# Kernel optimization log

Hardware: AMD Instinct MI355X
Metric: run time of the kernel (lower is better)

Reference implementation:

```python
import jax, jax.numpy as jnp
import numpy as np

DIM = 256
HEADS = 4
DEPTH = DIM // HEADS
EXPAND = 4
EPS = 1e-3  # keras BatchNormalization default epsilon


def _bn(x, gamma, beta, mean, var):
    # inference-mode batch norm over last axis
    return gamma * (x - mean) * jax.lax.rsqrt(var + EPS) + beta


def setup_inputs() -> dict:
    key = jax.random.key(0)
    ks = jax.random.split(key, 12)
    B, S, D = 4, 2048, DIM
    H = D * EXPAND
    s = 1.0 / np.sqrt(D)
    inp = {
        "x": jax.random.normal(ks[0], (B, S, D), jnp.float32),
        "bn1_gamma": jnp.ones((D,), jnp.float32),
        "bn1_beta": jnp.zeros((D,), jnp.float32),
        "bn1_mean": jax.random.normal(ks[1], (D,), jnp.float32) * 0.1,
        "bn1_var": jnp.abs(jax.random.normal(ks[2], (D,), jnp.float32)) + 0.5,
        "wq": jax.random.normal(ks[3], (D, D), jnp.float32) * s,
        "bq": jnp.zeros((D,), jnp.float32),
        "wk": jax.random.normal(ks[4], (D, D), jnp.float32) * s,
        "bk": jnp.zeros((D,), jnp.float32),
        "wv": jax.random.normal(ks[5], (D, D), jnp.float32) * s,
        "bv": jnp.zeros((D,), jnp.float32),
        "wo": jax.random.normal(ks[6], (D, D), jnp.float32) * s,
        "bo": jnp.zeros((D,), jnp.float32),
        "bn2_gamma": jnp.ones((D,), jnp.float32),
        "bn2_beta": jnp.zeros((D,), jnp.float32),
        "bn2_mean": jax.random.normal(ks[7], (D,), jnp.float32) * 0.1,
        "bn2_var": jnp.abs(jax.random.normal(ks[8], (D,), jnp.float32)) + 0.5,
        "w1": jax.random.normal(ks[9], (D, H), jnp.float32) * s,
        "w2": jax.random.normal(ks[10], (H, D), jnp.float32) * (1.0 / np.sqrt(H)),
    }
    return inp


def reference(x, bn1_gamma, bn1_beta, bn1_mean, bn1_var,
              wq, bq, wk, bk, wv, bv, wo, bo,
              bn2_gamma, bn2_beta, bn2_mean, bn2_var, w1, w2):
    B, S, D = x.shape
    h = _bn(x, bn1_gamma, bn1_beta, bn1_mean, bn1_var)
    # project and split heads -> [B, H, S, depth]
    def heads(t):
        return t.reshape(B, S, HEADS, DEPTH).transpose(0, 2, 1, 3)
    q = heads(h @ wq + bq)
    k = heads(h @ wk + bk)
    v = heads(h @ wv + bv)
    scores = jnp.einsum("bhqd,bhkd->bhqk", q, k) / jnp.sqrt(jnp.float32(DEPTH))
    attn = jax.nn.softmax(scores, axis=-1)
    ctx = jnp.einsum("bhqk,bhkd->bhqd", attn, v)
    ctx = ctx.transpose(0, 2, 1, 3).reshape(B, S, D)
    attn_out = ctx @ wo + bo
    x1 = attn_out + x  # residual (dropout = identity at inference)
    h2 = _bn(x1, bn2_gamma, bn2_beta, bn2_mean, bn2_var)
    m = jax.nn.gelu(h2 @ w1, approximate=False) @ w2
    return m + x1
```

## Files before the change

kernel.cpp:

```cpp
#include <hip/hip_runtime.h>

typedef unsigned short u16;
typedef unsigned int u32;
typedef short short8 __attribute__((ext_vector_type(8)));
typedef short short4v __attribute__((ext_vector_type(4)));
typedef float f32x4 __attribute__((ext_vector_type(4)));

#define EPS 1e-3f
#define C1F 0.18033688011112042f

#if defined(__HIP_DEVICE_COMPILE__)
#define MFMA16(a, b, c) __builtin_amdgcn_mfma_f32_16x16x16bf16_1k(a, b, c, 0, 0, 0)
#define EXP2F(x) __builtin_amdgcn_exp2f(x)
#else
#define MFMA16(a, b, c) (c)
#define EXP2F(x) exp2f(x)
#endif

static __device__ __forceinline__ u16 f2bf(float f) {
    u32 u = __float_as_uint(f);
    u += 0x7fffu + ((u >> 16) & 1u);
    return (u16)(u >> 16);
}
static __device__ __forceinline__ float bf2f(u16 v) {
    u32 u = (u32)v << 16;
    return __uint_as_float(u);
}
static __device__ __forceinline__ u32 pack_bf2_trunc(float a, float b) {
    return __builtin_amdgcn_perm(__float_as_uint(b), __float_as_uint(a), 0x07060302u);
}
static __device__ __forceinline__ void async_cp16(const void* g, void* l) {
    __builtin_amdgcn_global_load_lds(
        (const __attribute__((address_space(1))) unsigned int*)g,
        (__attribute__((address_space(3))) unsigned int*)l, 16, 0, 0);
}

__global__ void prep_bn1_kernel(const float* __restrict__ x,
                            const float* __restrict__ wq, const float* __restrict__ wk,
                            const float* __restrict__ wv, const float* __restrict__ wo,
                            const float* __restrict__ w1, const float* __restrict__ w2,
                            const float* __restrict__ bq, const float* __restrict__ bk,
                            const float* __restrict__ bv,
                            const float* __restrict__ g1, const float* __restrict__ b1,
                            const float* __restrict__ m1, const float* __restrict__ v1,
                            const float* __restrict__ g2, const float* __restrict__ b2,
                            const float* __restrict__ m2, const float* __restrict__ v2,
                            u16* __restrict__ h,
                            u16* __restrict__ wqkvT, u16* __restrict__ woT,
                            u16* __restrict__ w1T, u16* __restrict__ w2T,
                            float* __restrict__ bqkv,
                            float* __restrict__ bn2sc, float* __restrict__ bn2sh) {
    int bid = blockIdx.x;
    if (bid < 2048) {
        int idx = bid * 256 + threadIdx.x;
        int base = idx * 4;
        int c = base & 255;
        float4 xv = *(const float4*)(x + base);
        ushort4 pk;
        {
            float sc0 = g1[c] * rsqrtf(v1[c] + EPS);
            pk.x = f2bf(fmaf(xv.x, sc0, b1[c] - m1[c] * sc0));
            float sc1 = g1[c+1] * rsqrtf(v1[c+1] + EPS);
            pk.y = f2bf(fmaf(xv.y, sc1, b1[c+1] - m1[c+1] * sc1));
            float sc2 = g1[c+2] * rsqrtf(v1[c+2] + EPS);
            pk.z = f2bf(fmaf(xv.z, sc2, b1[c+2] - m1[c+2] * sc2));
            float sc3 = g1[c+3] * rsqrtf(v1[c+3] + EPS);
            pk.w = f2bf(fmaf(xv.w, sc3, b1[c+3] - m1[c+3] * sc3));
        }
        *(ushort4*)(h + base) = pk;
        return;
    }
    int idx = (bid - 2048) * 256 + threadIdx.x;
    if (idx < 196608) {
        int sec = idx >> 16;
        int i = idx & 65535;
        int k = i >> 8, n = i & 255;
        const float* w = sec == 0 ? wq : (sec == 1 ? wk : wv);
        float v = w[i];
        if (sec == 1) v *= C1F;
        wqkvT[(sec * 256 + n) * 256 + k] = f2bf(v);
    } else if (idx < 262144) {
        int i = idx - 196608; int k = i >> 8, n = i & 255;
        woT[n * 256 + k] = f2bf(wo[i]);
    } else if (idx < 524288) {
        int i = idx - 262144; int k = i >> 10, n = i & 1023;
        w1T[n * 256 + k] = f2bf(w1[i]);
    } else if (idx < 786432) {
        int i = idx - 524288; int k = i >> 8, n = i & 255;
        w2T[n * 1024 + k] = f2bf(w2[i]);
    } else if (idx < 787200) {
        int i = idx - 786432;
        bqkv[i] = (i < 256) ? bq[i] : (i < 512 ? bk[i - 256] * C1F : bv[i - 512]);
    } else if (idx < 787456) {
        int i = idx - 787200;
        float sc = g2[i] * rsqrtf(v2[i] + EPS);
        bn2sc[i] = sc; bn2sh[i] = b2[i] - m2[i] * sc;
    }
}

template <int EPI>
__global__ __launch_bounds__(256) void gemm128(
        const u16* __restrict__ A, const u16* __restrict__ Bt,
        int M, int N, int K,
        const float* __restrict__ bias, u16* __restrict__ out_bf,
        u16* __restrict__ out_vt) {
    __shared__ u16 abuf[2][4096];
    __shared__ u16 bbuf[2][8192];
    const int t = threadIdx.x;
    const int w = t >> 6, lane = t & 63;
    const int l = lane & 15, Q = lane >> 4;
    const int m0 = blockIdx.x * 64;
    const int n0 = blockIdx.y * 128;
    const int rh = (w & 1) * 32;
    const int ch = (w >> 1) * 64;

    f32x4 acc[2][4];
#pragma unroll
    for (int mt = 0; mt < 2; ++mt)
#pragma unroll
        for (int nt = 0; nt < 4; ++nt) acc[mt][nt] = (f32x4){0.f, 0.f, 0.f, 0.f};

    auto stage = [&](int k0, int b) {
#pragma unroll
        for (int j = 0; j < 2; ++j) {
            int idx = j * 256 + t;
            int r = idx >> 3, c8 = idx & 7;
            int sc = c8 ^ (r & 7);
            async_cp16(A + (size_t)(m0 + r) * K + k0 + sc * 8, abuf[b] + idx * 8);
        }
#pragma unroll
        for (int j = 0; j < 4; ++j) {
            int idx = j * 256 + t;
            int r = idx >> 3, c8 = idx & 7;
            int sc = c8 ^ (r & 7);
            async_cp16(Bt + (size_t)(n0 + r) * K + k0 + sc * 8, bbuf[b] + idx * 8);
        }
    };

    const int nit = K >> 6;
    stage(0, 0);
    for (int i = 0; i < nit; ++i) {
        __syncthreads();
        if (i + 1 < nit) stage((i + 1) << 6, (i + 1) & 1);
        const u16* ab = abuf[i & 1];
        const u16* bb = bbuf[i & 1];
#pragma unroll
        for (int kd = 0; kd < 2; ++kd) {
            short8 afr[2], bfr[4];
#pragma unroll
            for (int mt = 0; mt < 2; ++mt) {
                int ar = rh + mt * 16 + l;
                afr[mt] = *(const short8*)(ab + ar * 64 + (((kd * 4 + Q) ^ (ar & 7))) * 8);
            }
#pragma unroll
            for (int nt = 0; nt < 4; ++nt) {
                int br = ch + nt * 16 + l;
                bfr[nt] = *(const short8*)(bb + br * 64 + (((kd * 4 + Q) ^ (br & 7))) * 8);
            }
#pragma unroll
            for (int mt = 0; mt < 2; ++mt)
#pragma unroll
                for (int nt = 0; nt < 4; ++nt)
                    acc[mt][nt] = __builtin_amdgcn_mfma_f32_16x16x32_bf16(afr[mt], bfr[nt], acc[mt][nt], 0, 0, 0);
        }
    }

#pragma unroll
    for (int mt = 0; mt < 2; ++mt)
#pragma unroll
        for (int nt = 0; nt < 4; ++nt) {
            int col = n0 + ch + nt * 16 + l;
            int row0 = m0 + rh + mt * 16 + Q * 4;
            if (EPI == 0) {
                float b = bias[col];
                if (col < 512) {
#pragma unroll
                    for (int r = 0; r < 4; ++r)
                        out_bf[(size_t)(row0 + r) * 512 + col] = f2bf(acc[mt][nt][r] + b);
                } else {
                    ushort4 pk;
                    pk.x = f2bf(acc[mt][nt][0] + b);
                    pk.y = f2bf(acc[mt][nt][1] + b);
                    pk.z = f2bf(acc[mt][nt][2] + b);
                    pk.w = f2bf(acc[mt][nt][3] + b);
                    *(ushort4*)(out_vt + (size_t)(col - 512) * 8192 + row0) = pk;
                }
            } else {
#pragma unroll
                for (int r = 0; r < 4; ++r) {
                    float val = acc[mt][nt][r];
                    float gl = 0.5f * val * (1.f + erff(val * 0.70710678118654752f));
                    out_bf[(size_t)(row0 + r) * N + col] = f2bf(gl);
                }
            }
        }
}

__global__ __launch_bounds__(256) void gemm64_res(
        const u16* __restrict__ A, const u16* __restrict__ Bt,
        int M, int N, int K,
        const float* __restrict__ resid, float* __restrict__ out_f32) {
    __shared__ u16 abuf[2][4096];
    __shared__ u16 bbuf[2][4096];
    const int t = threadIdx.x;
    const int w = t >> 6, lane = t & 63;
    const int l = lane & 15, Q = lane >> 4;
    const int m0 = blockIdx.x * 64;
    const int n0 = blockIdx.y * 64;

    f32x4 acc[4];
#pragma unroll
    for (int nt = 0; nt < 4; ++nt) acc[nt] = (f32x4){0.f, 0.f, 0.f, 0.f};

    auto stage = [&](int k0, int b) {
#pragma unroll
        for (int j = 0; j < 2; ++j) {
            int idx = j * 256 + t;
            int r = idx >> 3, c8 = idx & 7;
            int sc = c8 ^ (r & 7);
            async_cp16(A + (size_t)(m0 + r) * K + k0 + sc * 8, abuf[b] + idx * 8);
        }
#pragma unroll
        for (int j = 0; j < 2; ++j) {
            int idx = j * 256 + t;
            int r = idx >> 3, c8 = idx & 7;
            int sc = c8 ^ (r & 7);
            async_cp16(Bt + (size_t)(n0 + r) * K + k0 + sc * 8, bbuf[b] + idx * 8);
        }
    };

    const int nit = K >> 6;
    stage(0, 0);
    for (int i = 0; i < nit; ++i) {
        __syncthreads();
        if (i + 1 < nit) stage((i + 1) << 6, (i + 1) & 1);
        const u16* ab = abuf[i & 1];
        const u16* bb = bbuf[i & 1];
#pragma unroll
        for (int kd = 0; kd < 2; ++kd) {
            int ar = w * 16 + l;
            short8 afr = *(const short8*)(ab + ar * 64 + (((kd * 4 + Q) ^ (ar & 7))) * 8);
#pragma unroll
            for (int nt = 0; nt < 4; ++nt) {
                int r = nt * 16 + l;
                short8 bfr = *(const short8*)(bb + r * 64 + (((kd * 4 + Q) ^ (r & 7))) * 8);
                acc[nt] = __builtin_amdgcn_mfma_f32_16x16x32_bf16(afr, bfr, acc[nt], 0, 0, 0);
            }
        }
    }

#pragma unroll
    for (int nt = 0; nt < 4; ++nt) {
        int col = n0 + nt * 16 + l;
        int row0 = m0 + w * 16 + Q * 4;
#pragma unroll
        for (int r = 0; r < 4; ++r) {
            size_t oidx = (size_t)(row0 + r) * N + col;
            out_f32[oidx] = acc[nt][r] + resid[oidx];
        }
    }
}

__global__ __launch_bounds__(256) void gemm_oproj(
        const u16* __restrict__ opart, const float* __restrict__ lpart,
        const u16* __restrict__ Bt,
        const float* __restrict__ bias, const float* __restrict__ resid,
        float* __restrict__ out_f32, u16* __restrict__ out_bf,
        const float* __restrict__ b2sc, const float* __restrict__ b2sh) {
    __shared__ u16 abuf[4096];
    __shared__ u16 bbuf[2][4096];
    const int t = threadIdx.x;
    const int w = t >> 6, lane = t & 63;
    const int l = lane & 15, Q = lane >> 4;
    const int m0 = blockIdx.x * 64;
    const int n0 = blockIdx.y * 64;
    const size_t SPSTR = (size_t)16 * 2048 * 64;

    f32x4 acc[4];
#pragma unroll
    for (int nt = 0; nt < 4; ++nt) acc[nt] = (f32x4){0.f, 0.f, 0.f, 0.f};

    auto stageB = [&](int k0, int b) {
#pragma unroll
        for (int j = 0; j < 2; ++j) {
            int idx = j * 256 + t;
            int r = idx >> 3, c8 = idx & 7;
            int sc = c8 ^ (r & 7);
            async_cp16(Bt + (size_t)(n0 + r) * 256 + k0 + sc * 8, bbuf[b] + idx * 8);
        }
    };

    stageB(0, 0);
    for (int i = 0; i < 4; ++i) {
        uint4 aw[2];
#pragma unroll
        for (int j = 0; j < 2; ++j) {
            int idx = j * 256 + t;
            int r = idx >> 3, c8 = idx & 7;
            int dc = c8 ^ (r & 7);
            int row = m0 + r;
            int bh = (row >> 11) * 4 + i;
            int q = row & 2047;
            size_t lb = (size_t)bh * 2048 + q;
            float ls = lpart[lb] + lpart[lb + 32768] + lpart[lb + 65536] + lpart[lb + 98304];
            float inv = 1.0f / ls;
            size_t base = ((size_t)bh * 2048 + q) * 64 + dc * 8;
            uint4 v0 = *(const uint4*)(opart + base);
            uint4 v1 = *(const uint4*)(opart + SPSTR + base);
            uint4 v2 = *(const uint4*)(opart + 2 * SPSTR + base);
            uint4 v3 = *(const uint4*)(opart + 3 * SPSTR + base);
            u32 o[4];
            const u32* p0 = &v0.x; const u32* p1 = &v1.x;
            const u32* p2 = &v2.x; const u32* p3 = &v3.x;
#pragma unroll
            for (int e = 0; e < 4; ++e) {
                float lo = __uint_as_float(p0[e] << 16) + __uint_as_float(p1[e] << 16)
                         + __uint_as_float(p2[e] << 16) + __uint_as_float(p3[e] << 16);
                float hi = __uint_as_float(p0[e] & 0xffff0000u) + __uint_as_float(p1[e] & 0xffff0000u)
                         + __uint_as_float(p2[e] & 0xffff0000u) + __uint_as_float(p3[e] & 0xffff0000u);
                o[e] = (u32)f2bf(lo * inv) | ((u32)f2bf(hi * inv) << 16);
            }
            aw[j] = make_uint4(o[0], o[1], o[2], o[3]);
        }
        __syncthreads();
#pragma unroll
        for (int j = 0; j < 2; ++j)
            *(uint4*)(abuf + ((size_t)(j * 256 + t)) * 8) = aw[j];
        if (i < 3) stageB((i + 1) * 64, (i + 1) & 1);
        __syncthreads();
        const u16* bb = bbuf[i & 1];
#pragma unroll
        for (int kd = 0; kd < 2; ++kd) {
            int ar = w * 16 + l;
            short8 afr = *(const short8*)(abuf + ar * 64 + (((kd * 4 + Q) ^ (ar & 7))) * 8);
#pragma unroll
            for (int nt = 0; nt < 4; ++nt) {
                int r = nt * 16 + l;
                short8 bfr = *(const short8*)(bb + r * 64 + (((kd * 4 + Q) ^ (r & 7))) * 8);
                acc[nt] = __builtin_amdgcn_mfma_f32_16x16x32_bf16(afr, bfr, acc[nt], 0, 0, 0);
            }
        }
    }

#pragma unroll
    for (int nt = 0; nt < 4; ++nt) {
        int col = n0 + nt * 16 + l;
        int row0 = m0 + w * 16 + Q * 4;
#pragma unroll
        for (int r = 0; r < 4; ++r) {
            size_t oidx = (size_t)(row0 + r) * 256 + col;
            float val = acc[nt][r] + bias[col] + resid[oidx];
            out_f32[oidx] = val;
            out_bf[oidx] = f2bf(fmaf(val, b2sc[col], b2sh[col]));
        }
    }
}

static __device__ __forceinline__ void stage_tiles(const u16* kglob, const u16* vglob,
                                                   u16* kdst, u16* vdst,
                                                   int w, int lane, int kt) {
#pragma unroll
    for (int j = 0; j < 2; ++j) {
        int cw = (w * 2 + j) * 64 + lane;
        int r = cw >> 3;
        int c = (cw & 7) ^ (r & 7);
        async_cp16(kglob + ((size_t)(kt * 64 + r)) * 512 + c * 8, kdst + (w * 2 + j) * 512);
        async_cp16(vglob + ((size_t)r) * 8192 + kt * 64 + c * 8, vdst + (w * 2 + j) * 512);
    }
}

__global__ __launch_bounds__(256) void attn_kernel(const u16* __restrict__ qk,
                                                   const u16* __restrict__ vT,
                                                   u16* __restrict__ opart,
                                                   float* __restrict__ lpart) {
    __shared__ u16 kbuf[4096];
    __shared__ u16 vbuf[4096];
    const int t = threadIdx.x;
    const int w = t >> 6, lane = t & 63;
    const int l = lane & 15, Q = lane >> 4;
    const int blk = blockIdx.x;
    const int qt = blk >> 6;
    const int sp = (blk >> 4) & 3;
    const int bh = blk & 15;
    const int bb = bh >> 2, hd = bh & 3;
    const size_t rowbase = (size_t)bb * 2048;
    const int q0 = qt * 64 + w * 16;

    short8 qf[2];
#pragma unroll
    for (int kd = 0; kd < 2; ++kd)
        qf[kd] = *(const short8*)(qk + (rowbase + q0 + l) * 512
                                  + hd * 64 + kd * 32 + Q * 8);

    f32x4 o[4];
#pragma unroll
    for (int dt = 0; dt < 4; ++dt) o[dt] = (f32x4){0.f, 0.f, 0.f, 0.f};
    f32x4 oL = (f32x4){0.f, 0.f, 0.f, 0.f};
    union { u32 u[2]; short4v s4; } ones;
    ones.u[0] = 0x3F803F80u; ones.u[1] = 0x3F803F80u;

    const u16* kglob = qk + (rowbase + sp * 512) * 512 + 256 + hd * 64;
    const u16* vglob = vT + ((size_t)(hd * 64)) * 8192 + rowbase + sp * 512;

    for (int kt = 0; kt < 8; ++kt) {
        stage_tiles(kglob, vglob, kbuf, vbuf, w, lane, kt);
        __syncthreads();

        union { u32 u[2]; short4v s4; } pf[4];
#pragma unroll
        for (int st = 0; st < 4; ++st) {
            int r = st * 16 + l;
            short8 kf0 = *(const short8*)(kbuf + r * 64 + ((Q) ^ (r & 7)) * 8);
            short8 kf1 = *(const short8*)(kbuf + r * 64 + ((4 + Q) ^ (r & 7)) * 8);
            f32x4 s = (f32x4){0.f, 0.f, 0.f, 0.f};
            s = __builtin_amdgcn_mfma_f32_16x16x32_bf16(kf0, qf[0], s, 0, 0, 0);
            s = __builtin_amdgcn_mfma_f32_16x16x32_bf16(kf1, qf[1], s, 0, 0, 0);
            float p0 = EXP2F(s[0]);
            float p1 = EXP2F(s[1]);
            float p2 = EXP2F(s[2]);
            float p3 = EXP2F(s[3]);
            pf[st].u[0] = pack_bf2_trunc(p0, p1);
            pf[st].u[1] = pack_bf2_trunc(p2, p3);
        }

#pragma unroll
        for (int c = 0; c < 4; ++c) {
#pragma unroll
            for (int dt = 0; dt < 4; ++dt) {
                int r = dt * 16 + l;
                int slot = (2 * c + (Q >> 1)) ^ (r & 7);
                short4v vf = *(const short4v*)(vbuf + r * 64 + slot * 8 + (Q & 1) * 4);
                o[dt] = MFMA16(vf, pf[c].s4, o[dt]);
            }
            oL = MFMA16(ones.s4, pf[c].s4, oL);
        }
        __syncthreads();
    }

    u16* ob = opart + (((size_t)sp * 16 + bh) * 2048 + q0) * 64;
#pragma unroll
    for (int dt = 0; dt < 4; ++dt) {
        ushort4 pk;
        pk.x = f2bf(o[dt][0]);
        pk.y = f2bf(o[dt][1]);
        pk.z = f2bf(o[dt][2]);
        pk.w = f2bf(o[dt][3]);
        *(ushort4*)(ob + (size_t)l * 64 + dt * 16 + Q * 4) = pk;
    }
    if (Q == 0) {
        size_t lb = ((size_t)sp * 16 + bh) * 2048 + q0;
        lpart[lb + l] = oL[0];
    }
}

extern "C" void kernel_launch(void* const* d_in, const int* in_sizes, int n_in,
                              void* d_out, int out_size, void* d_ws, size_t ws_size,
                              hipStream_t stream) {
    (void)in_sizes; (void)n_in; (void)out_size; (void)ws_size;
    const float* x  = (const float*)d_in[0];
    const float* g1 = (const float*)d_in[1];
    const float* b1 = (const float*)d_in[2];
    const float* m1 = (const float*)d_in[3];
    const float* v1 = (const float*)d_in[4];
    const float* wq = (const float*)d_in[5];
    const float* bq = (const float*)d_in[6];
    const float* wk = (const float*)d_in[7];
    const float* bk = (const float*)d_in[8];
    const float* wv = (const float*)d_in[9];
    const float* bv = (const float*)d_in[10];
    const float* wo = (const float*)d_in[11];
    const float* bo = (const float*)d_in[12];
    const float* g2 = (const float*)d_in[13];
    const float* b2 = (const float*)d_in[14];
    const float* m2 = (const float*)d_in[15];
    const float* v2 = (const float*)d_in[16];
    const float* w1 = (const float*)d_in[17];
    const float* w2 = (const float*)d_in[18];

    char* ws = (char*)d_ws;
    u16*   qkb    = (u16*)(ws + (0ull << 20));
    u16*   vTb    = (u16*)(ws + (8ull << 20));
    u16*   h_buf  = (u16*)(ws + (12ull << 20));
    float* x1     = (float*)(ws + (20ull << 20));
    u16*   h2     = (u16*)(ws + (28ull << 20));
    u16*   gbuf   = (u16*)(ws + (32ull << 20));
    u16*   opart  = (u16*)(ws + (48ull << 20));
    float* lpart  = (float*)(ws + (80ull << 20));
    u16*   wqkvT  = (u16*)(ws + (81ull << 20));
    u16*   woT    = (u16*)(ws + (82ull << 20));
    u16*   w1T    = (u16*)(ws + (83ull << 20));
    u16*   w2T    = (u16*)(ws + (84ull << 20));
    float* bqkv   = (float*)(ws + (85ull << 20));
    float* bn2sc  = (float*)(ws + (85ull << 20) + 4096);
    float* bn2sh  = (float*)(ws + (85ull << 20) + 8192);
    float* out    = (float*)d_out;

    prep_bn1_kernel<<<5125, 256, 0, stream>>>(x, wq, wk, wv, wo, w1, w2, bq, bk, bv,
                                              g1, b1, m1, v1, g2, b2, m2, v2,
                                              h_buf, wqkvT, woT, w1T, w2T, bqkv,
                                              bn2sc, bn2sh);
    gemm128<0><<<dim3(128, 6), 256, 0, stream>>>(
        h_buf, wqkvT, 8192, 768, 256, bqkv, qkb, vTb);
    attn_kernel<<<2048, 256, 0, stream>>>(qkb, vTb, opart, lpart);
    gemm_oproj<<<dim3(128, 4), 256, 0, stream>>>(
        opart, lpart, woT, bo, x, x1, h2, bn2sc, bn2sh);
    gemm128<2><<<dim3(128, 8), 256, 0, stream>>>(
        h2, w1T, 8192, 1024, 256, nullptr, gbuf, nullptr);
    gemm64_res<<<dim3(128, 4), 256, 0, stream>>>(
        gbuf, w2T, 8192, 256, 1024, x1, out);
}
```

Measured before the change: 176.7 us.

## Double-buffer K/V tiles and process two query groups per wave in attention

The attention kernel now has each wave handle 32 query rows (two 16-row groups) instead of 16, so every K/V fragment read from shared memory feeds twice as many MFMAs, and the grid is halved to 1024 blocks. K/V staging is double-buffered: the next tile's async copy is issued right after the barrier, overlapping with compute on the current tile, and the trailing barrier is removed. This cuts LDS traffic and exposed load latency, at the cost of more registers, double the shared memory and fewer blocks. The FFN GEMM launch now receives the bqkv pointer in place of nullptr, an unrelated change that may alter behaviour if that template path reads the bias.

```diff
diff --git a/kernel.cpp b/kernel.cpp
--- a/kernel.cpp
+++ b/kernel.cpp
@@ -373,8 +373,8 @@
                                                    const u16* __restrict__ vT,
                                                    u16* __restrict__ opart,
                                                    float* __restrict__ lpart) {
-    __shared__ u16 kbuf[4096];
-    __shared__ u16 vbuf[4096];
+    __shared__ u16 kbuf[2][4096];
+    __shared__ u16 vbuf[2][4096];
     const int t = threadIdx.x;
     const int w = t >> 6, lane = t & 63;
     const int l = lane & 15, Q = lane >> 4;
@@ -384,43 +384,57 @@
     const int bh = blk & 15;
     const int bb = bh >> 2, hd = bh & 3;
     const size_t rowbase = (size_t)bb * 2048;
-    const int q0 = qt * 64 + w * 16;
-
-    short8 qf[2];
-#pragma unroll
-    for (int kd = 0; kd < 2; ++kd)
-        qf[kd] = *(const short8*)(qk + (rowbase + q0 + l) * 512
-                                  + hd * 64 + kd * 32 + Q * 8);
-
-    f32x4 o[4];
-#pragma unroll
-    for (int dt = 0; dt < 4; ++dt) o[dt] = (f32x4){0.f, 0.f, 0.f, 0.f};
-    f32x4 oL = (f32x4){0.f, 0.f, 0.f, 0.f};
+    const int q0 = qt * 128 + w * 32;
+
+    short8 qf[2][2];
+#pragma unroll
+    for (int g = 0; g < 2; ++g)
+#pragma unroll
+        for (int kd = 0; kd < 2; ++kd)
+            qf[g][kd] = *(const short8*)(qk + (rowbase + q0 + g * 16 + l) * 512
+                                         + hd * 64 + kd * 32 + Q * 8);
+
+    f32x4 o[2][4];
+#pragma unroll
+    for (int g = 0; g < 2; ++g)
+#pragma unroll
+        for (int dt = 0; dt < 4; ++dt) o[g][dt] = (f32x4){0.f, 0.f, 0.f, 0.f};
+    f32x4 oL[2];
+    oL[0] = (f32x4){0.f, 0.f, 0.f, 0.f};
+    oL[1] = (f32x4){0.f, 0.f, 0.f, 0.f};
     union { u32 u[2]; short4v s4; } ones;
     ones.u[0] = 0x3F803F80u; ones.u[1] = 0x3F803F80u;
 
     const u16* kglob = qk + (rowbase + sp * 512) * 512 + 256 + hd * 64;
     const u16* vglob = vT + ((size_t)(hd * 64)) * 8192 + rowbase + sp * 512;
 
+    stage_tiles(kglob, vglob, kbuf[0], vbuf[0], w, lane, 0);
     for (int kt = 0; kt < 8; ++kt) {
-        stage_tiles(kglob, vglob, kbuf, vbuf, w, lane, kt);
         __syncthreads();
-
-        union { u32 u[2]; short4v s4; } pf[4];
+        if (kt + 1 < 8)
+            stage_tiles(kglob, vglob, kbuf[(kt + 1) & 1], vbuf[(kt + 1) & 1],
+                        w, lane, kt + 1);
+        const u16* kb = kbuf[kt & 1];
+        const u16* vb = vbuf[kt & 1];
+
+        union { u32 u[2]; short4v s4; } pf[2][4];
 #pragma unroll
         for (int st = 0; st < 4; ++st) {
             int r = st * 16 + l;
-            short8 kf0 = *(const short8*)(kbuf + r * 64 + ((Q) ^ (r & 7)) * 8);
-            short8 kf1 = *(const short8*)(kbuf + r * 64 + ((4 + Q) ^ (r & 7)) * 8);
-            f32x4 s = (f32x4){0.f, 0.f, 0.f, 0.f};
-            s = __builtin_amdgcn_mfma_f32_16x16x32_bf16(kf0, qf[0], s, 0, 0, 0);
-            s = __builtin_amdgcn_mfma_f32_16x16x32_bf16(kf1, qf[1], s, 0, 0, 0);
-            float p0 = EXP2F(s[0]);
-            float p1 = EXP2F(s[1]);
-            float p2 = EXP2F(s[2]);
-            float p3 = EXP2F(s[3]);
-            pf[st].u[0] = pack_bf2_trunc(p0, p1);
-            pf[st].u[1] = pack_bf2_trunc(p2, p3);
+            short8 kf0 = *(const short8*)(kb + r * 64 + ((Q) ^ (r & 7)) * 8);
+            short8 kf1 = *(const short8*)(kb + r * 64 + ((4 + Q) ^ (r & 7)) * 8);
+#pragma unroll
+            for (int g = 0; g < 2; ++g) {
+                f32x4 s = (f32x4){0.f, 0.f, 0.f, 0.f};
+                s = __builtin_amdgcn_mfma_f32_16x16x32_bf16(kf0, qf[g][0], s, 0, 0, 0);
+                s = __builtin_amdgcn_mfma_f32_16x16x32_bf16(kf1, qf[g][1], s, 0, 0, 0);
+                float p0 = EXP2F(s[0]);
+                float p1 = EXP2F(s[1]);
+                float p2 = EXP2F(s[2]);
+                float p3 = EXP2F(s[3]);
+                pf[g][st].u[0] = pack_bf2_trunc(p0, p1);
+                pf[g][st].u[1] = pack_bf2_trunc(p2, p3);
+            }
         }
 
 #pragma unroll
@@ -429,27 +443,31 @@
             for (int dt = 0; dt < 4; ++dt) {
                 int r = dt * 16 + l;
                 int slot = (2 * c + (Q >> 1)) ^ (r & 7);
-                short4v vf = *(const short4v*)(vbuf + r * 64 + slot * 8 + (Q & 1) * 4);
-                o[dt] = MFMA16(vf, pf[c].s4, o[dt]);
-            }
-            oL = MFMA16(ones.s4, pf[c].s4, oL);
-        }
-        __syncthreads();
-    }
-
-    u16* ob = opart + (((size_t)sp * 16 + bh) * 2048 + q0) * 64;
-#pragma unroll
-    for (int dt = 0; dt < 4; ++dt) {
-        ushort4 pk;
-        pk.x = f2bf(o[dt][0]);
-        pk.y = f2bf(o[dt][1]);
-        pk.z = f2bf(o[dt][2]);
-        pk.w = f2bf(o[dt][3]);
-        *(ushort4*)(ob + (size_t)l * 64 + dt * 16 + Q * 4) = pk;
-    }
-    if (Q == 0) {
-        size_t lb = ((size_t)sp * 16 + bh) * 2048 + q0;
-        lpart[lb + l] = oL[0];
+                short4v vf = *(const short4v*)(vb + r * 64 + slot * 8 + (Q & 1) * 4);
+                o[0][dt] = MFMA16(vf, pf[0][c].s4, o[0][dt]);
+                o[1][dt] = MFMA16(vf, pf[1][c].s4, o[1][dt]);
+            }
+            oL[0] = MFMA16(ones.s4, pf[0][c].s4, oL[0]);
+            oL[1] = MFMA16(ones.s4, pf[1][c].s4, oL[1]);
+        }
+    }
+
+#pragma unroll
+    for (int g = 0; g < 2; ++g) {
+        u16* ob = opart + (((size_t)sp * 16 + bh) * 2048 + q0 + g * 16) * 64;
+#pragma unroll
+        for (int dt = 0; dt < 4; ++dt) {
+            ushort4 pk;
+            pk.x = f2bf(o[g][dt][0]);
+            pk.y = f2bf(o[g][dt][1]);
+            pk.z = f2bf(o[g][dt][2]);
+            pk.w = f2bf(o[g][dt][3]);
+            *(ushort4*)(ob + (size_t)l * 64 + dt * 16 + Q * 4) = pk;
+        }
+        if (Q == 0) {
+            size_t lb = ((size_t)sp * 16 + bh) * 2048 + q0 + g * 16;
+            lpart[lb + l] = oL[g][0];
+        }
     }
 }
 
@@ -501,11 +519,11 @@
                                               bn2sc, bn2sh);
     gemm128<0><<<dim3(128, 6), 256, 0, stream>>>(
         h_buf, wqkvT, 8192, 768, 256, bqkv, qkb, vTb);
-    attn_kernel<<<2048, 256, 0, stream>>>(qkb, vTb, opart, lpart);
+    attn_kernel<<<1024, 256, 0, stream>>>(qkb, vTb, opart, lpart);
     gemm_oproj<<<dim3(128, 4), 256, 0, stream>>>(
         opart, lpart, woT, bo, x, x1, h2, bn2sc, bn2sh);
     gemm128<2><<<dim3(128, 8), 256, 0, stream>>>(
-        h2, w1T, 8192, 1024, 256, nullptr, gbuf, nullptr);
+        h2, w1T, 8192, 1024, 256, bqkv, gbuf, nullptr);
     gemm64_res<<<dim3(128, 4), 256, 0, stream>>>(
         gbuf, w2T, 8192, 256, 1024, x1, out);
 }
```

New measurement: 178.3 us. About the same (+0.9%).

## Retile output projection to 16-row blocks covering all 256 columns

Applied to the files above, without the earlier changes.

The output-projection GEMM now gives each block 16 rows and the full 256 output columns, one 64-column slice per wave, instead of 64x64 tiles on a 2D grid. Before, the split-K reduction of the attention partials (four partial sums plus normalisation) was recomputed once per column tile, four times in total. Now it runs once per row, which cuts redundant reads of opart and lpart. The cost is that every block stages the whole 256x64 weight slice per k-step (64KB of LDS for double buffering), which lowers occupancy, and only half the threads do the A-side work. The gemm128<2> call also now receives bqkv instead of a null pointer, which looks unrelated and may change that kernel's bias handling.

```diff
diff --git a/kernel.cpp b/kernel.cpp
--- a/kernel.cpp
+++ b/kernel.cpp
@@ -267,13 +267,12 @@
         const float* __restrict__ bias, const float* __restrict__ resid,
         float* __restrict__ out_f32, u16* __restrict__ out_bf,
         const float* __restrict__ b2sc, const float* __restrict__ b2sh) {
-    __shared__ u16 abuf[4096];
-    __shared__ u16 bbuf[2][4096];
+    __shared__ u16 abuf[1024];
+    __shared__ u16 bbuf[2][16384];
     const int t = threadIdx.x;
     const int w = t >> 6, lane = t & 63;
     const int l = lane & 15, Q = lane >> 4;
-    const int m0 = blockIdx.x * 64;
-    const int n0 = blockIdx.y * 64;
+    const int m0 = blockIdx.x * 16;
     const size_t SPSTR = (size_t)16 * 2048 * 64;
 
     f32x4 acc[4];
@@ -282,21 +281,19 @@
 
     auto stageB = [&](int k0, int b) {
 #pragma unroll
-        for (int j = 0; j < 2; ++j) {
+        for (int j = 0; j < 8; ++j) {
             int idx = j * 256 + t;
             int r = idx >> 3, c8 = idx & 7;
             int sc = c8 ^ (r & 7);
-            async_cp16(Bt + (size_t)(n0 + r) * 256 + k0 + sc * 8, bbuf[b] + idx * 8);
+            async_cp16(Bt + (size_t)r * 256 + k0 + sc * 8, bbuf[b] + idx * 8);
         }
     };
 
     stageB(0, 0);
     for (int i = 0; i < 4; ++i) {
-        uint4 aw[2];
-#pragma unroll
-        for (int j = 0; j < 2; ++j) {
-            int idx = j * 256 + t;
-            int r = idx >> 3, c8 = idx & 7;
+        uint4 aw;
+        if (t < 128) {
+            int r = t >> 3, c8 = t & 7;
             int dc = c8 ^ (r & 7);
             int row = m0 + r;
             int bh = (row >> 11) * 4 + i;
@@ -320,22 +317,20 @@
                          + __uint_as_float(p2[e] & 0xffff0000u) + __uint_as_float(p3[e] & 0xffff0000u);
                 o[e] = (u32)f2bf(lo * inv) | ((u32)f2bf(hi * inv) << 16);
             }
-            aw[j] = make_uint4(o[0], o[1], o[2], o[3]);
+            aw = make_uint4(o[0], o[1], o[2], o[3]);
         }
         __syncthreads();
-#pragma unroll
-        for (int j = 0; j < 2; ++j)
-            *(uint4*)(abuf + ((size_t)(j * 256 + t)) * 8) = aw[j];
+        if (t < 128)
+            *(uint4*)(abuf + (size_t)t * 8) = aw;
         if (i < 3) stageB((i + 1) * 64, (i + 1) & 1);
         __syncthreads();
         const u16* bb = bbuf[i & 1];
 #pragma unroll
         for (int kd = 0; kd < 2; ++kd) {
-            int ar = w * 16 + l;
-            short8 afr = *(const short8*)(abuf + ar * 64 + (((kd * 4 + Q) ^ (ar & 7))) * 8);
+            short8 afr = *(const short8*)(abuf + l * 64 + (((kd * 4 + Q) ^ (l & 7))) * 8);
 #pragma unroll
             for (int nt = 0; nt < 4; ++nt) {
-                int r = nt * 16 + l;
+                int r = w * 64 + nt * 16 + l;
                 short8 bfr = *(const short8*)(bb + r * 64 + (((kd * 4 + Q) ^ (r & 7))) * 8);
                 acc[nt] = __builtin_amdgcn_mfma_f32_16x16x32_bf16(afr, bfr, acc[nt], 0, 0, 0);
             }
@@ -344,8 +339,8 @@
 
 #pragma unroll
     for (int nt = 0; nt < 4; ++nt) {
-        int col = n0 + nt * 16 + l;
-        int row0 = m0 + w * 16 + Q * 4;
+        int col = w * 64 + nt * 16 + l;
+        int row0 = m0 + Q * 4;
 #pragma unroll
         for (int r = 0; r < 4; ++r) {
             size_t oidx = (size_t)(row0 + r) * 256 + col;
@@ -502,10 +497,10 @@
     gemm128<0><<<dim3(128, 6), 256, 0, stream>>>(
         h_buf, wqkvT, 8192, 768, 256, bqkv, qkb, vTb);
     attn_kernel<<<2048, 256, 0, stream>>>(qkb, vTb, opart, lpart);
-    gemm_oproj<<<dim3(128, 4), 256, 0, stream>>>(
+    gemm_oproj<<<512, 256, 0, stream>>>(
         opart, lpart, woT, bo, x, x1, h2, bn2sc, bn2sh);
     gemm128<2><<<dim3(128, 8), 256, 0, stream>>>(
-        h2, w1T, 8192, 1024, 256, nullptr, gbuf, nullptr);
+        h2, w1T, 8192, 1024, 256, bqkv, gbuf, nullptr);
     gemm64_res<<<dim3(128, 4), 256, 0, stream>>>(
         gbuf, w2T, 8192, 256, 1024, x1, out);
 }
```

After: 180.3 us. 2.1% more time.
